# Performance work log

Measured on AMD Instinct MI355X. Metric: run time of the kernel, lower is better.

The kernel has to match this reference:

```python
import jax, jax.numpy as jnp
import numpy as np

N = 50000        # nodes
E = 800000       # edges (avg degree 16)
F_IN = 11        # raw node features
HID = 128        # hidden_dim
HEADS = 4
C = HID // HEADS # per-head channels = 32
L = 4            # num_layers
NEG_SLOPE = 0.2  # PyG GATv2 default


def setup_inputs() -> dict:
    key = jax.random.key(0)
    ks = jax.random.split(key, 10)
    s = 0.1
    node_features = jax.random.normal(ks[0], (N, F_IN), jnp.float32)
    edge_index = jax.random.randint(ks[1], (2, E), 0, N, dtype=jnp.int32)
    W_emb = jax.random.normal(ks[2], (HID, F_IN), jnp.float32) * s
    b_emb = jnp.zeros((HID,), jnp.float32)
    Wl = jax.random.normal(ks[3], (L, HID, HID), jnp.float32) * s
    bl = jnp.zeros((L, HID), jnp.float32)
    Wr = jax.random.normal(ks[4], (L, HID, HID), jnp.float32) * s
    br = jnp.zeros((L, HID), jnp.float32)
    att = jax.random.normal(ks[5], (L, HEADS, C), jnp.float32) * s
    bias = jnp.zeros((L, HID), jnp.float32)
    return {
        "node_features": node_features, "edge_index": edge_index, "num_nodes": N,
        "W_emb": W_emb, "b_emb": b_emb, "Wl": Wl, "bl": bl,
        "Wr": Wr, "br": br, "att": att, "bias": bias,
    }


def _gatv2_layer(x, src, dst, Wl, bl, Wr, br, att, bias):
    """PyG GATv2Conv (concat=True, share_weights=False), dropout off."""
    n = x.shape[0]
    xl = (x @ Wl.T + bl).reshape(n, HEADS, C)  # source transform
    xr = (x @ Wr.T + br).reshape(n, HEADS, C)  # target transform
    e = jax.nn.leaky_relu(xl[src] + xr[dst], NEG_SLOPE)       # [E,H,C]
    logits = jnp.einsum('ehc,hc->eh', e, att)                 # [E,H]
    # segment softmax over incoming edges per destination node
    m = jax.ops.segment_max(logits, dst, num_segments=n)      # [N,H]
    m = jnp.where(jnp.isfinite(m), m, jnp.zeros_like(m))      # empty segments
    p = jnp.exp(logits - m[dst])                              # [E,H]
    denom = jax.ops.segment_sum(p, dst, num_segments=n)       # [N,H]
    alpha = p / denom[dst]
    out = jax.ops.segment_sum(alpha[:, :, None] * xl[src], dst, num_segments=n)
    return out.reshape(n, HID) + bias


def reference(node_features, edge_index, num_nodes, W_emb, b_emb, Wl, bl, Wr, br, att, bias):
    src, dst = edge_index[0], edge_index[1]
    x = jax.nn.relu(node_features @ W_emb.T + b_emb)
    for i in range(L):  # BatchNorms exist in the torch module but are never applied
        x_res = x
        x = _gatv2_layer(x, src, dst, Wl[i], bl[i], Wr[i], br[i], att[i], bias[i])
        x = jax.nn.relu(x)
        if i > 0:
            x = x + x_res
    graph_mean = jnp.mean(x, axis=0)
    graph_max = jnp.max(x, axis=0)
    graph_embedding = jnp.concatenate([graph_mean, graph_max], axis=-1)  # [2*HID]
    return graph_embedding, x
```

## Files before the change

### kernel.cpp

```cpp
#include <hip/hip_runtime.h>
#include <math.h>

#define HID 128
#define HEADS 4
#define NEG_SLOPE 0.2f
#define R1B 1024
#define BCAP 8192
#define PB 6144
#define ACHUNK 4096

typedef float f32x4 __attribute__((ext_vector_type(4)));
typedef _Float16 f16x8 __attribute__((ext_vector_type(8)));
typedef _Float16 f16x4 __attribute__((ext_vector_type(4)));
typedef _Float16 f16x2 __attribute__((ext_vector_type(2)));

#if defined(__has_builtin)
#if __has_builtin(__builtin_amdgcn_fdot2)
#define HAVE_FDOT2 1
#endif
#endif


__global__ __launch_bounds__(256) void k_binA(const int* __restrict__ src, const int* __restrict__ dst,
                                              int E, int* __restrict__ gcnt, int* __restrict__ arena) {
    __shared__ int lh[256];
    __shared__ int lbase[256];
    __shared__ unsigned short lrank[ACHUNK];
    const int tid = threadIdx.x;
    lh[tid] = 0;
    __syncthreads();
    const int e0 = blockIdx.x * ACHUNK;
    #pragma unroll
    for (int i = 0; i < ACHUNK / 256; i++) {
        int e = e0 + i * 256 + tid;
        if (e < E) {
            int b = dst[e] >> 8;
            lrank[i * 256 + tid] = (unsigned short)atomicAdd(&lh[b], 1);
        }
    }
    __syncthreads();
    if (lh[tid] > 0) lbase[tid] = atomicAdd(&gcnt[tid], lh[tid]);
    __syncthreads();
    #pragma unroll
    for (int i = 0; i < ACHUNK / 256; i++) {
        int e = e0 + i * 256 + tid;
        if (e < E) {
            int d = dst[e];
            int b = d >> 8;
            arena[b * BCAP + lbase[b] + lrank[i * 256 + tid]] = (src[e] << 8) | (d & 255);
        }
    }
}

__global__ __launch_bounds__(256) void k_binB(const int* __restrict__ arena, const int* __restrict__ gcnt,
                                              int N, int E,
                                              int* __restrict__ rowptr, int* __restrict__ csr_off) {
    __shared__ int ncnt[256];
    __shared__ int sbuf[256];
    __shared__ int nstart[256];
    __shared__ int exv[256];
    __shared__ int stage[PB];
    __shared__ unsigned short rk[BCAP];
    const int b = blockIdx.x, tid = threadIdx.x;

    int gv = gcnt[tid];
    sbuf[tid] = gv;
    __syncthreads();
    for (int off = 1; off < 256; off <<= 1) {
        int t = (tid >= off) ? sbuf[tid - off] : 0;
        __syncthreads();
        sbuf[tid] += t;
        __syncthreads();
    }
    exv[tid] = sbuf[tid] - gv;
    if (b == 0 && tid == 0) rowptr[N] = E;
    __syncthreads();
    const int seg = exv[b];
    const int cnt = gcnt[b];

    ncnt[tid] = 0;
    __syncthreads();
    for (int k = tid; k < cnt; k += 256) {
        int v = arena[b * BCAP + k];
        rk[k] = (unsigned short)atomicAdd(&ncnt[v & 255], 1);
    }
    __syncthreads();
    int c = ncnt[tid];
    sbuf[tid] = c;
    __syncthreads();
    for (int off = 1; off < 256; off <<= 1) {
        int t = (tid >= off) ? sbuf[tid - off] : 0;
        __syncthreads();
        sbuf[tid] += t;
        __syncthreads();
    }
    int myStart = sbuf[tid] - c;
    nstart[tid] = myStart;
    int n = b * 256 + tid;
    if (n < N) rowptr[n] = seg + myStart;
    __syncthreads();
    for (int k = tid; k < cnt; k += 256) {
        int v = arena[b * BCAP + k];
        int pos = nstart[v & 255] + rk[k];
        int val = v & 0xFFFFFF00;
        if (pos < PB) stage[pos] = val;
        else          csr_off[seg + pos] = val;
    }
    __syncthreads();
    int lim = min(cnt, PB);
    for (int k = tid; k < lim; k += 256) csr_off[seg + k] = stage[k];
}


__device__ inline f16x2 absh2(f16x2 v) {
    unsigned u = __builtin_bit_cast(unsigned, v) & 0x7FFF7FFFu;
    return __builtin_bit_cast(f16x2, u);
}

__device__ inline f16x8 zero8() {
    f16x8 z;
    #pragma unroll
    for (int i = 0; i < 8; i++) z[i] = (_Float16)0.f;
    return z;
}

template <int CTRL>
__device__ inline float qp_xor_add(float x) {
    int y = __builtin_amdgcn_update_dpp(0, __builtin_bit_cast(int, x),
                                        CTRL, 0xF, 0xF, true);
    return x + __builtin_bit_cast(float, y);
}

__device__ inline float edge_logit8(f16x8 c,
                                    f16x2 xr0, f16x2 xr1, f16x2 xr2, f16x2 xr3,
                                    f16x2 a0, f16x2 a1, f16x2 a2, f16x2 a3) {
    const f16x2 k06 = (f16x2){(_Float16)0.6f, (_Float16)0.6f};
    const f16x2 k04 = (f16x2){(_Float16)0.4f, (_Float16)0.4f};
    f16x2 c0 = __builtin_shufflevector(c, c, 0, 1);
    f16x2 c1 = __builtin_shufflevector(c, c, 2, 3);
    f16x2 c2 = __builtin_shufflevector(c, c, 4, 5);
    f16x2 c3 = __builtin_shufflevector(c, c, 6, 7);
    f16x2 u0 = c0 + xr0, u1 = c1 + xr1, u2 = c2 + xr2, u3 = c3 + xr3;
    f16x2 l0 = u0 * k06 + absh2(u0) * k04;
    f16x2 l1 = u1 * k06 + absh2(u1) * k04;
    f16x2 l2 = u2 * k06 + absh2(u2) * k04;
    f16x2 l3 = u3 * k06 + absh2(u3) * k04;
#ifdef HAVE_FDOT2
    float p = __builtin_amdgcn_fdot2(l0, a0, 0.f, false);
    p = __builtin_amdgcn_fdot2(l1, a1, p, false);
    p = __builtin_amdgcn_fdot2(l2, a2, p, false);
    p = __builtin_amdgcn_fdot2(l3, a3, p, false);
#else
    float p = (float)l0[0] * (float)a0[0] + (float)l0[1] * (float)a0[1]
            + (float)l1[0] * (float)a1[0] + (float)l1[1] * (float)a1[1]
            + (float)l2[0] * (float)a2[0] + (float)l2[1] * (float)a2[1]
            + (float)l3[0] * (float)a3[0] + (float)l3[1] * (float)a3[1];
#endif
    return p;
}

#define ACC_ROW(WP, R)                                                        \
    acc16[0] += (WP) * __builtin_shufflevector((R), (R), 0, 1);               \
    acc16[1] += (WP) * __builtin_shufflevector((R), (R), 2, 3);               \
    acc16[2] += (WP) * __builtin_shufflevector((R), (R), 4, 5);               \
    acc16[3] += (WP) * __builtin_shufflevector((R), (R), 6, 7);

__global__ __launch_bounds__(256) void k_tof16(const float* __restrict__ a, const float* __restrict__ b,
                                               _Float16* __restrict__ oa, _Float16* __restrict__ ob,
                                               int* __restrict__ gcnt, int n) {
    if (blockIdx.x == 0 && blockIdx.y == 0) gcnt[threadIdx.x] = 0;
    const float* x = blockIdx.y ? b : a;
    _Float16*    o = blockIdx.y ? ob : oa;
    int base = (blockIdx.x * 256 + threadIdx.x) * 4;
    if (base >= n) return;
    float4 v = *(const float4*)(x + base);
    f16x4 h = {(_Float16)v.x, (_Float16)v.y, (_Float16)v.z, (_Float16)v.w};
    *(f16x4*)(o + base) = h;
}


__global__ __launch_bounds__(512) void k_linear_mfma(
        const _Float16* __restrict__ xh,
        const _Float16* __restrict__ WfL, const _Float16* __restrict__ WfR,
        const float* __restrict__ bl, const float* __restrict__ br,
        _Float16* __restrict__ xlh, _Float16* __restrict__ xrh, int N) {
    __shared__ _Float16 lds[17408];
    const int t   = threadIdx.x;
    const int mat = blockIdx.y;
    const _Float16* W = mat ? WfR : WfL;

    for (int g = t; g < 2048; g += 512) {
        int r = g >> 4, cc = g & 15;
        int dsto = r * 128 + ((cc ^ (r & 7)) << 3);
        *(float4*)&lds[dsto] = *(const float4*)(W + g * 8);
    }
    __syncthreads();

    const int wave = t >> 6;
    const int lane = t & 63;
    const int l16  = lane & 15;
    const int quad = lane >> 4;
    const int n0   = blockIdx.x * 256 + wave * 32;

    int arow0 = n0 + l16;
    int arow1 = n0 + 16 + l16;
    if (arow0 >= N) arow0 = N - 1;
    if (arow1 >= N) arow1 = N - 1;

    f32x4 acc[2][8];
    #pragma unroll
    for (int u = 0; u < 2; u++)
        #pragma unroll
        for (int s = 0; s < 8; s++) acc[u][s] = (f32x4){0.f, 0.f, 0.f, 0.f};

    #pragma unroll
    for (int k0 = 0; k0 < HID; k0 += 32) {
        f16x8 a0 = *(const f16x8*)(xh + arow0 * HID + k0 + quad * 8);
        f16x8 a1 = *(const f16x8*)(xh + arow1 * HID + k0 + quad * 8);
        const int cc = (k0 >> 3) + quad;
        #pragma unroll
        for (int s = 0; s < 8; s++) {
            const int row = s * 16 + l16;
            const int off = row * 128 + ((cc ^ (l16 & 7)) << 3);
            f16x8 b = *(const f16x8*)&lds[off];
            acc[0][s] = __builtin_amdgcn_mfma_f32_16x16x32_f16(a0, b, acc[0][s], 0, 0, 0);
            acc[1][s] = __builtin_amdgcn_mfma_f32_16x16x32_f16(a1, b, acc[1][s], 0, 0, 0);
        }
    }

    const float* bias = mat ? br : bl;
    _Float16* dst = mat ? xrh : xlh;
    const int wl = wave & 3;

    #pragma unroll
    for (int round = 0; round < 2; round++) {
        __syncthreads();
        if ((wave >> 2) == round) {
            #pragma unroll
            for (int s = 0; s < 8; s++) {
                int col = s * 16 + l16;
                float bv = bias[col];
                #pragma unroll
                for (int u = 0; u < 2; u++) {
                    #pragma unroll
                    for (int r = 0; r < 4; r++) {
                        int nd = wl * 32 + u * 16 + quad * 4 + r;
                        lds[nd * 136 + col] = (_Float16)(acc[u][s][r] + bv);
                    }
                }
            }
        }
        __syncthreads();
        const int base_node = blockIdx.x * 256 + round * 128;
        #pragma unroll
        for (int it = 0; it < 4; it++) {
            int idx = it * 512 + t;
            int node = base_node + (idx >> 4);
            if (node < N)
                *(float4*)(dst + (size_t)node * HID + (idx & 15) * 8) =
                    *(float4*)&lds[(idx >> 4) * 136 + (idx & 15) * 8];
        }
    }
}


__global__ __launch_bounds__(256, 8) void k_attn(const _Float16* __restrict__ xlh, const _Float16* __restrict__ xrh,
                                              const int* __restrict__ rowptr, const int* __restrict__ csr_off,
                                              const float* __restrict__ att, const float* __restrict__ bias,
                                              const _Float16* __restrict__ xres, _Float16* __restrict__ outx,
                                              float* __restrict__ out,
                                              int add_res, int want_half, int N) {
    const int wave = threadIdx.x >> 6;
    const int lane = threadIdx.x & 63;
    const int strm = lane >> 4;
    const int l16  = lane & 15;
    const int n = blockIdx.x * 4 + wave;
    if (n >= N) return;

    const float4 aA = *(const float4*)(att + 8 * l16);
    const float4 aB = *(const float4*)(att + 8 * l16 + 4);
    const f16x2 a0 = (f16x2){(_Float16)aA.x, (_Float16)aA.y};
    const f16x2 a1 = (f16x2){(_Float16)aA.z, (_Float16)aA.w};
    const f16x2 a2 = (f16x2){(_Float16)aB.x, (_Float16)aB.y};
    const f16x2 a3 = (f16x2){(_Float16)aB.z, (_Float16)aB.w};
    const f16x8 xrv = *(const f16x8*)(xrh + (size_t)n * HID + 8 * l16);
    const f16x2 xr0 = __builtin_shufflevector(xrv, xrv, 0, 1);
    const f16x2 xr1 = __builtin_shufflevector(xrv, xrv, 2, 3);
    const f16x2 xr2 = __builtin_shufflevector(xrv, xrv, 4, 5);
    const f16x2 xr3 = __builtin_shufflevector(xrv, xrv, 6, 7);
    const int s0 = rowptr[n], s1 = rowptr[n + 1];
    const int deg = s1 - s0;

    float den = 0.f;
    f16x2 acc16[4];
    #pragma unroll
    for (int q = 0; q < 4; q++) acc16[q] = (f16x2){(_Float16)0.f, (_Float16)0.f};

    const char* xlb = (const char*)xlh + l16 * 16;
    const int j = s0 + 2 * strm;

    if (deg > 0 && deg <= 16) {
        const int last = s1 - 1;
        const int e0 = j, e1 = j + 1, e2 = j + 8, e3 = j + 9;
        f16x8 r0, r1, r2, r3;
        if (e0 < s1) {
            int o0 = csr_off[e0];
            int o1 = csr_off[min(e1, last)];
            r0 = *(const f16x8*)(xlb + o0);
            r1 = *(const f16x8*)(xlb + o1);
        } else { r0 = zero8(); r1 = zero8(); }
        if (e2 < s1) {
            int o2 = csr_off[e2];
            int o3 = csr_off[min(e3, last)];
            r2 = *(const f16x8*)(xlb + o2);
            r3 = *(const f16x8*)(xlb + o3);
        } else { r2 = zero8(); r3 = zero8(); }

        float p0 = edge_logit8(r0, xr0, xr1, xr2, xr3, a0, a1, a2, a3);
        float p1 = edge_logit8(r1, xr0, xr1, xr2, xr3, a0, a1, a2, a3);
        float p2 = edge_logit8(r2, xr0, xr1, xr2, xr3, a0, a1, a2, a3);
        float p3 = edge_logit8(r3, xr0, xr1, xr2, xr3, a0, a1, a2, a3);
        p0 = qp_xor_add<0xB1>(p0); p0 = qp_xor_add<0x4E>(p0);
        p1 = qp_xor_add<0xB1>(p1); p1 = qp_xor_add<0x4E>(p1);
        p2 = qp_xor_add<0xB1>(p2); p2 = qp_xor_add<0x4E>(p2);
        p3 = qp_xor_add<0xB1>(p3); p3 = qp_xor_add<0x4E>(p3);
        float w0 = (e0 < s1) ? __expf(p0) : 0.f;
        float w1 = (e1 < s1) ? __expf(p1) : 0.f;
        float w2 = (e2 < s1) ? __expf(p2) : 0.f;
        float w3 = (e3 < s1) ? __expf(p3) : 0.f;
        den += (w0 + w1) + (w2 + w3);
        f16x2 wp0 = (f16x2){(_Float16)w0, (_Float16)w0};
        f16x2 wp1 = (f16x2){(_Float16)w1, (_Float16)w1};
        f16x2 wp2 = (f16x2){(_Float16)w2, (_Float16)w2};
        f16x2 wp3 = (f16x2){(_Float16)w3, (_Float16)w3};
        ACC_ROW(wp0, r0)
        ACC_ROW(wp1, r1)
        ACC_ROW(wp2, r2)
        ACC_ROW(wp3, r3)
    } else if (deg > 16) {
        const int last = s1 - 1;
        int jj = j;
        f16x8 pa0 = *(const f16x8*)(xlb + csr_off[jj]);
        f16x8 pb0 = *(const f16x8*)(xlb + csr_off[jj + 1]);
        f16x8 pa1 = *(const f16x8*)(xlb + csr_off[jj + 8]);
        f16x8 pb1 = *(const f16x8*)(xlb + csr_off[jj + 9]);
        int oa = csr_off[min(jj + 16, last)];
        int ob = csr_off[min(jj + 17, last)];
        while (jj < s1) {
            f16x8 ca = pa0, cb = pb0;
            pa0 = pa1; pb0 = pb1;
            if (jj + 16 < s1) {
                pa1 = *(const f16x8*)(xlb + oa);
                pb1 = *(const f16x8*)(xlb + ob);
                oa = csr_off[min(jj + 24, last)];
                ob = csr_off[min(jj + 25, last)];
            } else { pa1 = zero8(); pb1 = zero8(); }

            float pa = edge_logit8(ca, xr0, xr1, xr2, xr3, a0, a1, a2, a3);
            float pb = edge_logit8(cb, xr0, xr1, xr2, xr3, a0, a1, a2, a3);
            pa = qp_xor_add<0xB1>(pa); pa = qp_xor_add<0x4E>(pa);
            pb = qp_xor_add<0xB1>(pb); pb = qp_xor_add<0x4E>(pb);
            float wa = __expf(pa);
            float wb = (jj + 1 < s1) ? __expf(pb) : 0.f;
            den += wa + wb;
            f16x2 wpa = (f16x2){(_Float16)wa, (_Float16)wa};
            f16x2 wpb = (f16x2){(_Float16)wb, (_Float16)wb};
            ACC_ROW(wpa, ca)
            ACC_ROW(wpb, cb)
            jj += 8;
        }
    }

    den += __shfl_xor(den, 16);
    den += __shfl_xor(den, 32);
    #pragma unroll
    for (int q = 0; q < 4; q++) {
        float pk = __builtin_bit_cast(float, acc16[q]);
        acc16[q] += __builtin_bit_cast(f16x2, __shfl_xor(pk, 16));
        pk = __builtin_bit_cast(float, acc16[q]);
        acc16[q] += __builtin_bit_cast(f16x2, __shfl_xor(pk, 32));
    }

    if (strm == 0) {
        float acc[8];
        #pragma unroll
        for (int q = 0; q < 4; q++) {
            acc[2 * q]     = (float)acc16[q][0];
            acc[2 * q + 1] = (float)acc16[q][1];
        }
        float4 bA = *(const float4*)(bias + 8 * l16);
        float4 bB = *(const float4*)(bias + 8 * l16 + 4);
        float b[8] = {bA.x, bA.y, bA.z, bA.w, bB.x, bB.y, bB.z, bB.w};
        float inv = (den > 0.f) ? 1.f / den : 0.f;
        float v[8];
        #pragma unroll
        for (int q = 0; q < 8; q++) v[q] = fmaxf(acc[q] * inv + b[q], 0.f);
        if (add_res) {
            f16x8 r = *(const f16x8*)(xres + (size_t)n * HID + 8 * l16);
            #pragma unroll
            for (int q = 0; q < 8; q++) v[q] += (float)r[q];
        }
        if (want_half) {
            f16x8 h;
            #pragma unroll
            for (int q = 0; q < 8; q++) h[q] = (_Float16)v[q];
            *(f16x8*)(outx + (size_t)n * HID + 8 * l16) = h;
        } else {
            *(float4*)(out + (size_t)n * HID + 8 * l16)     = make_float4(v[0], v[1], v[2], v[3]);
            *(float4*)(out + (size_t)n * HID + 8 * l16 + 4) = make_float4(v[4], v[5], v[6], v[7]);
        }
    }
}


__global__ __launch_bounds__(256) void k_embed(const float* __restrict__ nf, const float* __restrict__ W,
                                               const float* __restrict__ b,
                                               _Float16* __restrict__ xh, int N) {
    __shared__ float f[2][11];
    const int sub = threadIdx.x >> 7;
    const int h   = threadIdx.x & 127;
    const int n   = blockIdx.x * 2 + sub;
    if (n < N && h < 11) f[sub][h] = nf[(size_t)n * 11 + h];
    __syncthreads();
    if (n >= N) return;
    float acc = b[h];
    #pragma unroll
    for (int k = 0; k < 11; k++) acc += f[sub][k] * W[h * 11 + k];
    xh[(size_t)n * HID + h] = (_Float16)fmaxf(acc, 0.f);
}


__global__ __launch_bounds__(256) void k_reduce1(const float* __restrict__ x, int N,
                                                 float* __restrict__ psum, float* __restrict__ pmax) {
    __shared__ float ls[8][HID];
    __shared__ float lm[8][HID];
    const int c4 = (threadIdx.x & 31) << 2;
    const int rl = threadIdx.x >> 5;
    const int per = (N + gridDim.x - 1) / gridDim.x;
    const int n0 = blockIdx.x * per, n1 = min(N, n0 + per);
    float4 s = make_float4(0.f, 0.f, 0.f, 0.f);
    float4 m = make_float4(-INFINITY, -INFINITY, -INFINITY, -INFINITY);
    for (int n = n0 + rl; n < n1; n += 8) {
        float4 v = *(const float4*)(x + (size_t)n * HID + c4);
        s.x += v.x; s.y += v.y; s.z += v.z; s.w += v.w;
        m.x = fmaxf(m.x, v.x); m.y = fmaxf(m.y, v.y);
        m.z = fmaxf(m.z, v.z); m.w = fmaxf(m.w, v.w);
    }
    *(float4*)&ls[rl][c4] = s;
    *(float4*)&lm[rl][c4] = m;
    __syncthreads();
    if (rl < 4) {
        float4 a = *(float4*)&ls[rl][c4], bq = *(float4*)&ls[rl + 4][c4];
        a.x += bq.x; a.y += bq.y; a.z += bq.z; a.w += bq.w;
        *(float4*)&ls[rl][c4] = a;
        float4 am = *(float4*)&lm[rl][c4], bm = *(float4*)&lm[rl + 4][c4];
        am.x = fmaxf(am.x, bm.x); am.y = fmaxf(am.y, bm.y);
        am.z = fmaxf(am.z, bm.z); am.w = fmaxf(am.w, bm.w);
        *(float4*)&lm[rl][c4] = am;
    }
    __syncthreads();
    if (rl < 2) {
        float4 a = *(float4*)&ls[rl][c4], bq = *(float4*)&ls[rl + 2][c4];
        a.x += bq.x; a.y += bq.y; a.z += bq.z; a.w += bq.w;
        *(float4*)&ls[rl][c4] = a;
        float4 am = *(float4*)&lm[rl][c4], bm = *(float4*)&lm[rl + 2][c4];
        am.x = fmaxf(am.x, bm.x); am.y = fmaxf(am.y, bm.y);
        am.z = fmaxf(am.z, bm.z); am.w = fmaxf(am.w, bm.w);
        *(float4*)&lm[rl][c4] = am;
    }
    __syncthreads();
    if (rl == 0) {
        float4 a = *(float4*)&ls[0][c4], bq = *(float4*)&ls[1][c4];
        a.x += bq.x; a.y += bq.y; a.z += bq.z; a.w += bq.w;
        *(float4*)(psum + (size_t)blockIdx.x * HID + c4) = a;
        float4 am = *(float4*)&lm[0][c4], bm = *(float4*)&lm[1][c4];
        am.x = fmaxf(am.x, bm.x); am.y = fmaxf(am.y, bm.y);
        am.z = fmaxf(am.z, bm.z); am.w = fmaxf(am.w, bm.w);
        *(float4*)(pmax + (size_t)blockIdx.x * HID + c4) = am;
    }
}

__global__ __launch_bounds__(1024) void k_reduce2(const float* __restrict__ psum, const float* __restrict__ pmax,
                                                  int nb, float* __restrict__ out, float invN) {
    __shared__ float ss[8][HID];
    __shared__ float sm[8][HID];
    int h = threadIdx.x & 127;
    int c = threadIdx.x >> 7;
    int per = nb >> 3;
    float s = 0.f, m = -INFINITY;
    for (int b = c * per; b < (c + 1) * per; b++) {
        s += psum[b * HID + h];
        m = fmaxf(m, pmax[b * HID + h]);
    }
    ss[c][h] = s; sm[c][h] = m;
    __syncthreads();
    if (c < 4) { ss[c][h] += ss[c + 4][h]; sm[c][h] = fmaxf(sm[c][h], sm[c + 4][h]); }
    __syncthreads();
    if (c < 2) { ss[c][h] += ss[c + 2][h]; sm[c][h] = fmaxf(sm[c][h], sm[c + 2][h]); }
    __syncthreads();
    if (c == 0) {
        out[h] = (ss[0][h] + ss[1][h]) * invN;
        out[HID + h] = fmaxf(sm[0][h], sm[1][h]);
    }
}


extern "C" void kernel_launch(void* const* d_in, const int* in_sizes, int n_in,
                              void* d_out, int out_size, void* d_ws, size_t ws_size,
                              hipStream_t stream) {
    const float* nf    = (const float*)d_in[0];
    const int*   ei    = (const int*)d_in[1];
    const float* W_emb = (const float*)d_in[3];
    const float* b_emb = (const float*)d_in[4];
    const float* Wl    = (const float*)d_in[5];
    const float* bl    = (const float*)d_in[6];
    const float* Wr    = (const float*)d_in[7];
    const float* br    = (const float*)d_in[8];
    const float* att   = (const float*)d_in[9];
    const float* bias  = (const float*)d_in[10];

    const int N = in_sizes[0] / 11;
    const int E = in_sizes[1] / 2;
    const int* src = ei;
    const int* dst = ei + E;

    float* out  = (float*)d_out;
    float* xout = out + 2 * HID;

    char* w = (char*)d_ws;
    _Float16* xlh  = (_Float16*)w; w += (size_t)N * HID * 2;
    _Float16* xrh  = (_Float16*)w; w += (size_t)N * HID * 2;
    _Float16* xA   = (_Float16*)w; w += (size_t)N * HID * 2;
    _Float16* xB   = (_Float16*)w; w += (size_t)N * HID * 2;
    _Float16* WfL  = (_Float16*)w; w += (size_t)4 * HID * HID * 2;
    _Float16* WfR  = (_Float16*)w; w += (size_t)4 * HID * HID * 2;
    int*   gcnt    = (int*)w;   w += (size_t)256 * 4;
    int*   rowptr  = (int*)w;   w += (size_t)(N + 1) * 4;
    int*   arena   = (int*)w;   w += (size_t)256 * BCAP * 4;
    int*   csr_off = (int*)w;   w += (size_t)E * 4;
    float* psum    = (float*)w; w += (size_t)R1B * HID * 4;
    float* pmax    = (float*)w; w += (size_t)R1B * HID * 4;

    const int nbk = (N + 255) >> 8;
    const int nW = 4 * HID * HID;

    dim3 tg((nW / 4 + 255) / 256, 2);
    k_tof16<<<tg, 256, 0, stream>>>(Wl, Wr, WfL, WfR, gcnt, nW);

    k_binA<<<(E + ACHUNK - 1) / ACHUNK, 256, 0, stream>>>(src, dst, E, gcnt, arena);
    k_binB<<<nbk, 256, 0, stream>>>(arena, gcnt, N, E, rowptr, csr_off);

    k_embed<<<(N + 1) / 2, 256, 0, stream>>>(nf, W_emb, b_emb, xA, N);

    dim3 lgrid((N + 255) / 256, 2);
    for (int i = 0; i < 4; i++) {
        const _Float16* xin = (i & 1) ? xB : xA;
        _Float16* xo        = (i & 1) ? xA : xB;
        k_linear_mfma<<<lgrid, 512, 0, stream>>>(xin,
                                                 WfL + (size_t)i * HID * HID, WfR + (size_t)i * HID * HID,
                                                 bl + i * HID, br + i * HID, xlh, xrh, N);
        k_attn<<<(N + 3) / 4, 256, 0, stream>>>(xlh, xrh, rowptr, csr_off,
                                                att + i * HEADS * 32, bias + i * HID,
                                                xin, xo, xout,
                                                i > 0 ? 1 : 0, i < 3 ? 1 : 0, N);
    }

    k_reduce1<<<R1B, 256, 0, stream>>>(xout, N, psum, pmax);
    k_reduce2<<<1, 1024, 0, stream>>>(psum, pmax, R1B, out, 1.0f / N);
}
```

Baseline: 373.9 us.

## Fuse embed with weight conversion, widen single-shot attention path, halve reduce blocks

Merges the embedding kernel and the fp32-to-fp16 weight conversion into one launch, dropping a kernel launch. Extends the non-looping attention fast path from degree 16 to degree 24 by loading six neighbor rows per lane instead of four, so nodes with moderate degree avoid the pipelined loop. The number of partial-reduction blocks is also halved. The wider fast path raises register pressure and does wasted masked work for low-degree nodes.

```diff
diff --git a/kernel.cpp b/kernel.cpp
--- a/kernel.cpp
+++ b/kernel.cpp
@@ -4,7 +4,7 @@
 #define HID 128
 #define HEADS 4
 #define NEG_SLOPE 0.2f
-#define R1B 1024
+#define R1B 512
 #define BCAP 8192
 #define PB 6144
 #define ACHUNK 4096
@@ -165,17 +165,39 @@
     acc16[2] += (WP) * __builtin_shufflevector((R), (R), 4, 5);               \
     acc16[3] += (WP) * __builtin_shufflevector((R), (R), 6, 7);
 
-__global__ __launch_bounds__(256) void k_tof16(const float* __restrict__ a, const float* __restrict__ b,
-                                               _Float16* __restrict__ oa, _Float16* __restrict__ ob,
-                                               int* __restrict__ gcnt, int n) {
-    if (blockIdx.x == 0 && blockIdx.y == 0) gcnt[threadIdx.x] = 0;
-    const float* x = blockIdx.y ? b : a;
-    _Float16*    o = blockIdx.y ? ob : oa;
-    int base = (blockIdx.x * 256 + threadIdx.x) * 4;
-    if (base >= n) return;
-    float4 v = *(const float4*)(x + base);
-    f16x4 h = {(_Float16)v.x, (_Float16)v.y, (_Float16)v.z, (_Float16)v.w};
-    *(f16x4*)(o + base) = h;
+
+__global__ __launch_bounds__(256) void k_prep(const float* __restrict__ nf, const float* __restrict__ We,
+                                              const float* __restrict__ be, _Float16* __restrict__ xh,
+                                              int N,
+                                              const float* __restrict__ Wl, const float* __restrict__ Wr,
+                                              _Float16* __restrict__ WfL, _Float16* __restrict__ WfR,
+                                              int* __restrict__ gcnt, int nW) {
+    __shared__ float f[2][11];
+    const int nEmb = (N + 1) / 2;
+    const int bid = blockIdx.x;
+    if (bid < nEmb) {
+        const int sub = threadIdx.x >> 7;
+        const int h   = threadIdx.x & 127;
+        const int n   = bid * 2 + sub;
+        if (n < N && h < 11) f[sub][h] = nf[(size_t)n * 11 + h];
+        __syncthreads();
+        if (n >= N) return;
+        float acc = be[h];
+        #pragma unroll
+        for (int k = 0; k < 11; k++) acc += f[sub][k] * We[h * 11 + k];
+        xh[(size_t)n * HID + h] = (_Float16)fmaxf(acc, 0.f);
+    } else {
+        const int tb = bid - nEmb;
+        if (tb == 0) gcnt[threadIdx.x] = 0;
+        const int mat = tb >> 6;
+        const float* x = mat ? Wr : Wl;
+        _Float16*    o = mat ? WfR : WfL;
+        int base = ((tb & 63) * 256 + threadIdx.x) * 4;
+        if (base >= nW) return;
+        float4 v = *(const float4*)(x + base);
+        f16x4 h = {(_Float16)v.x, (_Float16)v.y, (_Float16)v.z, (_Float16)v.w};
+        *(f16x4*)(o + base) = h;
+    }
 }
 
 
@@ -299,45 +321,60 @@
     const char* xlb = (const char*)xlh + l16 * 16;
     const int j = s0 + 2 * strm;
 
-    if (deg > 0 && deg <= 16) {
+    if (deg > 0 && deg <= 24) {
         const int last = s1 - 1;
-        const int e0 = j, e1 = j + 1, e2 = j + 8, e3 = j + 9;
-        f16x8 r0, r1, r2, r3;
-        if (e0 < s1) {
-            int o0 = csr_off[e0];
-            int o1 = csr_off[min(e1, last)];
+        f16x8 r0, r1, r2, r3, r4, r5;
+        if (j < s1) {
+            int o0 = csr_off[j];
+            int o1 = csr_off[min(j + 1, last)];
             r0 = *(const f16x8*)(xlb + o0);
             r1 = *(const f16x8*)(xlb + o1);
         } else { r0 = zero8(); r1 = zero8(); }
-        if (e2 < s1) {
-            int o2 = csr_off[e2];
-            int o3 = csr_off[min(e3, last)];
+        if (j + 8 < s1) {
+            int o2 = csr_off[j + 8];
+            int o3 = csr_off[min(j + 9, last)];
             r2 = *(const f16x8*)(xlb + o2);
             r3 = *(const f16x8*)(xlb + o3);
         } else { r2 = zero8(); r3 = zero8(); }
+        if (j + 16 < s1) {
+            int o4 = csr_off[j + 16];
+            int o5 = csr_off[min(j + 17, last)];
+            r4 = *(const f16x8*)(xlb + o4);
+            r5 = *(const f16x8*)(xlb + o5);
+        } else { r4 = zero8(); r5 = zero8(); }
 
         float p0 = edge_logit8(r0, xr0, xr1, xr2, xr3, a0, a1, a2, a3);
         float p1 = edge_logit8(r1, xr0, xr1, xr2, xr3, a0, a1, a2, a3);
         float p2 = edge_logit8(r2, xr0, xr1, xr2, xr3, a0, a1, a2, a3);
         float p3 = edge_logit8(r3, xr0, xr1, xr2, xr3, a0, a1, a2, a3);
+        float p4 = edge_logit8(r4, xr0, xr1, xr2, xr3, a0, a1, a2, a3);
+        float p5 = edge_logit8(r5, xr0, xr1, xr2, xr3, a0, a1, a2, a3);
         p0 = qp_xor_add<0xB1>(p0); p0 = qp_xor_add<0x4E>(p0);
         p1 = qp_xor_add<0xB1>(p1); p1 = qp_xor_add<0x4E>(p1);
         p2 = qp_xor_add<0xB1>(p2); p2 = qp_xor_add<0x4E>(p2);
         p3 = qp_xor_add<0xB1>(p3); p3 = qp_xor_add<0x4E>(p3);
-        float w0 = (e0 < s1) ? __expf(p0) : 0.f;
-        float w1 = (e1 < s1) ? __expf(p1) : 0.f;
-        float w2 = (e2 < s1) ? __expf(p2) : 0.f;
-        float w3 = (e3 < s1) ? __expf(p3) : 0.f;
-        den += (w0 + w1) + (w2 + w3);
+        p4 = qp_xor_add<0xB1>(p4); p4 = qp_xor_add<0x4E>(p4);
+        p5 = qp_xor_add<0xB1>(p5); p5 = qp_xor_add<0x4E>(p5);
+        float w0 = (j      < s1) ? __expf(p0) : 0.f;
+        float w1 = (j + 1  < s1) ? __expf(p1) : 0.f;
+        float w2 = (j + 8  < s1) ? __expf(p2) : 0.f;
+        float w3 = (j + 9  < s1) ? __expf(p3) : 0.f;
+        float w4 = (j + 16 < s1) ? __expf(p4) : 0.f;
+        float w5 = (j + 17 < s1) ? __expf(p5) : 0.f;
+        den += (w0 + w1) + (w2 + w3) + (w4 + w5);
         f16x2 wp0 = (f16x2){(_Float16)w0, (_Float16)w0};
         f16x2 wp1 = (f16x2){(_Float16)w1, (_Float16)w1};
         f16x2 wp2 = (f16x2){(_Float16)w2, (_Float16)w2};
         f16x2 wp3 = (f16x2){(_Float16)w3, (_Float16)w3};
+        f16x2 wp4 = (f16x2){(_Float16)w4, (_Float16)w4};
+        f16x2 wp5 = (f16x2){(_Float16)w5, (_Float16)w5};
         ACC_ROW(wp0, r0)
         ACC_ROW(wp1, r1)
         ACC_ROW(wp2, r2)
         ACC_ROW(wp3, r3)
-    } else if (deg > 16) {
+        ACC_ROW(wp4, r4)
+        ACC_ROW(wp5, r5)
+    } else if (deg > 24) {
         const int last = s1 - 1;
         int jj = j;
         f16x8 pa0 = *(const f16x8*)(xlb + csr_off[jj]);
@@ -413,23 +450,6 @@
 }
 
 
-__global__ __launch_bounds__(256) void k_embed(const float* __restrict__ nf, const float* __restrict__ W,
-                                               const float* __restrict__ b,
-                                               _Float16* __restrict__ xh, int N) {
-    __shared__ float f[2][11];
-    const int sub = threadIdx.x >> 7;
-    const int h   = threadIdx.x & 127;
-    const int n   = blockIdx.x * 2 + sub;
-    if (n < N && h < 11) f[sub][h] = nf[(size_t)n * 11 + h];
-    __syncthreads();
-    if (n >= N) return;
-    float acc = b[h];
-    #pragma unroll
-    for (int k = 0; k < 11; k++) acc += f[sub][k] * W[h * 11 + k];
-    xh[(size_t)n * HID + h] = (_Float16)fmaxf(acc, 0.f);
-}
-
-
 __global__ __launch_bounds__(256) void k_reduce1(const float* __restrict__ x, int N,
                                                  float* __restrict__ psum, float* __restrict__ pmax) {
     __shared__ float ls[8][HID];
@@ -544,13 +564,12 @@
     const int nbk = (N + 255) >> 8;
     const int nW = 4 * HID * HID;
 
-    dim3 tg((nW / 4 + 255) / 256, 2);
-    k_tof16<<<tg, 256, 0, stream>>>(Wl, Wr, WfL, WfR, gcnt, nW);
+    const int nEmb = (N + 1) / 2;
+    k_prep<<<nEmb + 128, 256, 0, stream>>>(nf, W_emb, b_emb, xA, N,
+                                           Wl, Wr, WfL, WfR, gcnt, nW);
 
     k_binA<<<(E + ACHUNK - 1) / ACHUNK, 256, 0, stream>>>(src, dst, E, gcnt, arena);
     k_binB<<<nbk, 256, 0, stream>>>(arena, gcnt, N, E, rowptr, csr_off);
-
-    k_embed<<<(N + 1) / 2, 256, 0, stream>>>(nf, W_emb, b_emb, xA, N);
 
     dim3 lgrid((N + 255) / 256, 2);
     for (int i = 0; i < 4; i++) {
```

Result: faster. 362.8 us (-3.0%).
